# Performance work log

Hardware: AMD Instinct MI355X
Metric: run time of the kernel (lower is better)

Reference implementation:

```python
import jax, jax.numpy as jnp
import numpy as np

E = 8        # num_experts
D_IN = 512   # num_inputs
H = 256      # num_neurons_expert
T = 64       # num_neurons_tower
B = 16384    # batch


def setup_inputs() -> dict:
    key = jax.random.key(0)
    ks = jax.random.split(key, 7)
    s_in = 1.0 / np.sqrt(D_IN)
    s_h = 1.0 / np.sqrt(H)
    return {
        "xv": jax.random.normal(ks[0], (B, D_IN), dtype=jnp.float32),
        # expert weights stacked: torch Linear weight is (out,in) -> (E, H, D_IN)
        "We": jax.random.uniform(ks[1], (E, H, D_IN), jnp.float32, -s_in, s_in),
        "be": jax.random.uniform(ks[2], (E, H), jnp.float32, -s_in, s_in),
        "Wg": jax.random.uniform(ks[3], (E, D_IN), jnp.float32, -s_in, s_in),
        "bg": jax.random.uniform(ks[4], (E,), jnp.float32, -s_in, s_in),
        "Wt": jax.random.uniform(ks[5], (T, H), jnp.float32, -s_h, s_h),
        "bt": jax.random.uniform(ks[6], (T,), jnp.float32, -s_h, s_h),
    }


def reference(xv, We, be, Wg, bg, Wt, bt):
    # All experts as one batched GEMM: [B,D] x [E,H,D] -> [B,E,H]
    experts = jax.nn.relu(jnp.einsum("bd,ehd->beh", xv, We) + be[None, :, :])
    # Dropout is identity in eval mode.
    gate = jax.nn.softmax(xv @ Wg.T + bg, axis=1)            # [B,E]
    combined = jnp.einsum("beh,be->bh", experts, gate)        # [B,H]
    out = jax.nn.sigmoid(combined @ Wt.T + bt)                # [B,T]
    return out
```

## Files before the change

### kernel.cpp

```cpp
#include <hip/hip_runtime.h>
#include <hip/hip_bf16.h>
#include <stdint.h>

typedef unsigned short u16;
typedef __bf16 bf16x8 __attribute__((ext_vector_type(8)));
typedef float f32x4 __attribute__((ext_vector_type(4)));


__device__ __forceinline__ void glds16(const void* g, void* l) {
  __builtin_amdgcn_global_load_lds(
      (const __attribute__((address_space(1))) unsigned int*)g,
      (__attribute__((address_space(3))) unsigned int*)l, 16, 0, 0);
}

__device__ __forceinline__ u16 f2bf(float f) {
  unsigned int u = __builtin_bit_cast(unsigned int, f);
  u += 0x7fffu + ((u >> 16) & 1u);
  return (u16)(u >> 16);
}

__global__ __launch_bounds__(256) void prep_w(
    const float* __restrict__ We, const float* __restrict__ Wt,
    const float* __restrict__ Wg,
    u16* __restrict__ We_bf, u16* __restrict__ Wt_bf,
    u16* __restrict__ Wg_hi, u16* __restrict__ Wg_lo) {
  const int bx = blockIdx.x;
  if (bx < 520) {
    const float* src; u16* dst;
    if (bx < 512) { int base = bx * 2048 + threadIdx.x * 8; src = We + base; dst = We_bf + base; }
    else { int base = (bx - 512) * 2048 + threadIdx.x * 8; src = Wt + base; dst = Wt_bf + base; }
    float4 a = *(const float4*)src;
    float4 b = *(const float4*)(src + 4);
    uint4 o;
    o.x = (unsigned)f2bf(a.x) | ((unsigned)f2bf(a.y) << 16);
    o.y = (unsigned)f2bf(a.z) | ((unsigned)f2bf(a.w) << 16);
    o.z = (unsigned)f2bf(b.x) | ((unsigned)f2bf(b.y) << 16);
    o.w = (unsigned)f2bf(b.z) | ((unsigned)f2bf(b.w) << 16);
    *(uint4*)dst = o;
  } else {
    int base = (bx - 520) * 2048 + threadIdx.x * 8;
    float x[8];
    float4 a = *(const float4*)(Wg + base);
    float4 b = *(const float4*)(Wg + base + 4);
    x[0]=a.x; x[1]=a.y; x[2]=a.z; x[3]=a.w; x[4]=b.x; x[5]=b.y; x[6]=b.z; x[7]=b.w;
    u16 h[8], l[8];
#pragma unroll
    for (int j = 0; j < 8; j++) {
      h[j] = f2bf(x[j]);
      float hf = __builtin_bit_cast(float, ((unsigned)h[j]) << 16);
      l[j] = f2bf(x[j] - hf);
    }
    uint4 oh, ol;
    oh.x = (unsigned)h[0] | ((unsigned)h[1] << 16);
    oh.y = (unsigned)h[2] | ((unsigned)h[3] << 16);
    oh.z = (unsigned)h[4] | ((unsigned)h[5] << 16);
    oh.w = (unsigned)h[6] | ((unsigned)h[7] << 16);
    ol.x = (unsigned)l[0] | ((unsigned)l[1] << 16);
    ol.y = (unsigned)l[2] | ((unsigned)l[3] << 16);
    ol.z = (unsigned)l[4] | ((unsigned)l[5] << 16);
    ol.w = (unsigned)l[6] | ((unsigned)l[7] << 16);
    *(uint4*)(Wg_hi + base) = oh;
    *(uint4*)(Wg_lo + base) = ol;
  }
}

__device__ __forceinline__ void stage_chunk(const u16* __restrict__ We_bf,
                                            u16* ldsbuf, int t, int tid) {
  const int e_ = t >> 2, kc_ = t & 3;
  const u16* src = We_bf + (e_ << 17) + (kc_ << 7);
#pragma unroll
  for (int r = 0; r < 8; r++) {
    int gi = r * 512 + tid;
    int n = gi >> 4, s = gi & 15;
    int g = (s & 8) | ((s & 7) ^ (n & 7));
    glds16(src + (n << 9) + (g << 3), ldsbuf + (gi << 3));
  }
}

__global__ __launch_bounds__(512, 1) void moe_main(
    const float* __restrict__ xv, const u16* __restrict__ We_bf,
    const float* __restrict__ be, const float* __restrict__ bg,
    const u16* __restrict__ Wg_hi, const u16* __restrict__ Wg_lo,
    const u16* __restrict__ Wt_bf, const float* __restrict__ bt,
    float* __restrict__ out) {
  __shared__ u16 lds[65536];

  const int tid = threadIdx.x;
  const int lane = tid & 63;
  const int wid = tid >> 6;
  const int wm = wid >> 2;
  const int wn = wid & 3;
  const int l15 = lane & 15;
  const int l4 = lane >> 4;
  const int m0 = blockIdx.x << 6;

  stage_chunk(We_bf, lds, 0, tid);

  bf16x8 ah[2][16];
  f32x4 gacc[2] = {{0.f,0.f,0.f,0.f},{0.f,0.f,0.f,0.f}};
  const int esrc = l15 & 7;
#pragma unroll
  for (int mt = 0; mt < 2; mt++) {
#pragma unroll
    for (int ks = 0; ks < 16; ks++) {
      const float* ap = xv + ((m0 + wm * 32 + mt * 16 + l15) << 9) + ks * 32 + l4 * 8;
      float4 xa = *(const float4*)ap;
      float4 xb = *(const float4*)(ap + 4);
      float x[8];
      x[0]=xa.x; x[1]=xa.y; x[2]=xa.z; x[3]=xa.w; x[4]=xb.x; x[5]=xb.y; x[6]=xb.z; x[7]=xb.w;
      bf16x8 hv, lv;
#pragma unroll
      for (int j = 0; j < 8; j++) {
        u16 hb_ = f2bf(x[j]);
        float hf = __builtin_bit_cast(float, ((unsigned)hb_) << 16);
        hv[j] = __builtin_bit_cast(__bf16, hb_);
        lv[j] = __builtin_bit_cast(__bf16, f2bf(x[j] - hf));
      }
      ah[mt][ks] = hv;
      bf16x8 wh = *(const bf16x8*)(Wg_hi + (esrc << 9) + ks * 32 + l4 * 8);
      bf16x8 wl = *(const bf16x8*)(Wg_lo + (esrc << 9) + ks * 32 + l4 * 8);
      gacc[mt] = __builtin_amdgcn_mfma_f32_16x16x32_bf16(hv, wh, gacc[mt], 0, 0, 0);
      gacc[mt] = __builtin_amdgcn_mfma_f32_16x16x32_bf16(lv, wh, gacc[mt], 0, 0, 0);
      gacc[mt] = __builtin_amdgcn_mfma_f32_16x16x32_bf16(hv, wl, gacc[mt], 0, 0, 0);
    }
  }
  float gv[2][4];
  {
    float bgv = bg[esrc];
#pragma unroll
    for (int mt = 0; mt < 2; mt++)
#pragma unroll
      for (int i = 0; i < 4; i++) {
        float z = gacc[mt][i] + bgv;
        float mx = z;
        mx = fmaxf(mx, __shfl_xor(mx, 1));
        mx = fmaxf(mx, __shfl_xor(mx, 2));
        mx = fmaxf(mx, __shfl_xor(mx, 4));
        float p = __expf(z - mx);
        float s = p;
        s += __shfl_xor(s, 1);
        s += __shfl_xor(s, 2);
        s += __shfl_xor(s, 4);
        gv[mt][i] = p / s;
      }
  }

  f32x4 comb[2][4];
#pragma unroll
  for (int mt = 0; mt < 2; mt++)
#pragma unroll
    for (int nt = 0; nt < 4; nt++) comb[mt][nt] = {0.f, 0.f, 0.f, 0.f};

#pragma unroll 1
  for (int e = 0; e < 8; e++) {
    f32x4 acc[2][4];
#pragma unroll
    for (int mt = 0; mt < 2; mt++)
#pragma unroll
      for (int nt = 0; nt < 4; nt++) acc[mt][nt] = {0.f, 0.f, 0.f, 0.f};

#pragma unroll
    for (int kc = 0; kc < 4; kc++) {
      __syncthreads();
      int t = e * 4 + kc + 1;
      if (t < 32) stage_chunk(We_bf, &lds[(((kc & 1) ^ 1) << 15)], t, tid);
      const u16* ldsB = &lds[((kc & 1) << 15)];
#pragma unroll
      for (int ks = 0; ks < 4; ks++) {
        const int gg = ks * 4 + l4;
        bf16x8 bfr[4];
#pragma unroll
        for (int nt = 0; nt < 4; nt++) {
          int n = wn * 64 + nt * 16 + l15;
          int slot = (gg & 8) | ((gg & 7) ^ (n & 7));
          bfr[nt] = *(const bf16x8*)&ldsB[(n << 7) + (slot << 3)];
        }
#pragma unroll
        for (int mt = 0; mt < 2; mt++)
#pragma unroll
          for (int nt = 0; nt < 4; nt++)
            acc[mt][nt] = __builtin_amdgcn_mfma_f32_16x16x32_bf16(
                ah[mt][kc * 4 + ks], bfr[nt], acc[mt][nt], 0, 0, 0);
      }
    }
    float bev[4];
#pragma unroll
    for (int nt = 0; nt < 4; nt++)
      bev[nt] = be[(e << 8) + wn * 64 + nt * 16 + l15];
#pragma unroll
    for (int mt = 0; mt < 2; mt++)
#pragma unroll
      for (int i = 0; i < 4; i++) {
        float g = __shfl(gv[mt][i], (lane & 48) | e);
#pragma unroll
        for (int nt = 0; nt < 4; nt++)
          comb[mt][nt][i] += g * fmaxf(acc[mt][nt][i] + bev[nt], 0.f);
      }
  }

  __syncthreads();
#pragma unroll
  for (int mt = 0; mt < 2; mt++)
#pragma unroll
    for (int i = 0; i < 4; i++) {
      int row = wm * 32 + mt * 16 + l4 * 4 + i;
#pragma unroll
      for (int nt = 0; nt < 4; nt++) {
        int col = wn * 64 + nt * 16 + l15;
        __bf16 v = (__bf16)comb[mt][nt][i];
        lds[row * 264 + col] = __builtin_bit_cast(u16, v);
      }
    }
  __syncthreads();
  if (wid < 4) {
    f32x4 tacc[4];
#pragma unroll
    for (int nt = 0; nt < 4; nt++) tacc[nt] = {0.f, 0.f, 0.f, 0.f};
#pragma unroll
    for (int ks = 0; ks < 8; ks++) {
      bf16x8 aT = *(const bf16x8*)&lds[(wid * 16 + l15) * 264 + ks * 32 + l4 * 8];
#pragma unroll
      for (int nt = 0; nt < 4; nt++) {
        bf16x8 bT = *(const bf16x8*)&Wt_bf[(nt * 16 + l15) * 256 + ks * 32 + l4 * 8];
        tacc[nt] = __builtin_amdgcn_mfma_f32_16x16x32_bf16(aT, bT, tacc[nt], 0, 0, 0);
      }
    }
#pragma unroll
    for (int nt = 0; nt < 4; nt++) {
      float btv = bt[nt * 16 + l15];
#pragma unroll
      for (int i = 0; i < 4; i++) {
        int row = m0 + wid * 16 + l4 * 4 + i;
        float v = tacc[nt][i] + btv;
        out[row * 64 + nt * 16 + l15] = 1.f / (1.f + __expf(-v));
      }
    }
  }
}

extern "C" void kernel_launch(void* const* d_in, const int* in_sizes, int n_in,
                              void* d_out, int out_size, void* d_ws, size_t ws_size,
                              hipStream_t stream) {
  const float* xv = (const float*)d_in[0];
  const float* We = (const float*)d_in[1];
  const float* be = (const float*)d_in[2];
  const float* Wg = (const float*)d_in[3];
  const float* bg = (const float*)d_in[4];
  const float* Wt = (const float*)d_in[5];
  const float* bt = (const float*)d_in[6];

  char* ws = (char*)d_ws;
  u16* We_bf = (u16*)ws;
  u16* Wt_bf = (u16*)(ws + 2097152);
  u16* Wg_hi = (u16*)(ws + 2129920);
  u16* Wg_lo = (u16*)(ws + 2138112);

  prep_w<<<522, 256, 0, stream>>>(We, Wt, Wg, We_bf, Wt_bf, Wg_hi, Wg_lo);
  moe_main<<<256, 512, 0, stream>>>(xv, We_bf, be, bg, Wg_hi, Wg_lo, Wt_bf, bt,
                                    (float*)d_out);
}
```

Before: 157.6 us.

## Prefetch two weight chunks ahead with explicit waitcnt barriers, cache expert bias in LDS

Restructures the We chunk staging so each LDS buffer is refilled two chunks ahead, right after it is consumed. Explicit vmcnt waits and raw s_barriers replace the per-chunk __syncthreads, so global-to-LDS loads can overlap more MFMA work. The gate GEMM now uses three independent accumulators to break the MFMA dependency chain. The expert bias is also staged once into LDS instead of being read from global memory per expert. The hand-written waitcnt counts and the removal of the final sync carry a risk of race conditions if the counts are wrong.

```diff
diff --git a/kernel.cpp b/kernel.cpp
--- a/kernel.cpp
+++ b/kernel.cpp
@@ -6,6 +6,11 @@
 typedef __bf16 bf16x8 __attribute__((ext_vector_type(8)));
 typedef float f32x4 __attribute__((ext_vector_type(4)));
 
+
+#define SBAR __builtin_amdgcn_s_barrier()
+#define SCHEDB __builtin_amdgcn_sched_barrier(0)
+#define WAIT_V8 asm volatile("s_waitcnt vmcnt(8) lgkmcnt(0)" ::: "memory")
+#define WAIT_V0 asm volatile("s_waitcnt vmcnt(0) lgkmcnt(0)" ::: "memory")
 
 __device__ __forceinline__ void glds16(const void* g, void* l) {
   __builtin_amdgcn_global_load_lds(
@@ -83,7 +88,8 @@
     const u16* __restrict__ Wg_hi, const u16* __restrict__ Wg_lo,
     const u16* __restrict__ Wt_bf, const float* __restrict__ bt,
     float* __restrict__ out) {
-  __shared__ u16 lds[65536];
+  __shared__ u16 lds[69632];
+  float* beL = (float*)&lds[65536];
 
   const int tid = threadIdx.x;
   const int lane = tid & 63;
@@ -95,9 +101,13 @@
   const int m0 = blockIdx.x << 6;
 
   stage_chunk(We_bf, lds, 0, tid);
+  *(float4*)(beL + (tid << 2)) = *(const float4*)(be + (tid << 2));
+  stage_chunk(We_bf, &lds[32768], 1, tid);
 
   bf16x8 ah[2][16];
-  f32x4 gacc[2] = {{0.f,0.f,0.f,0.f},{0.f,0.f,0.f,0.f}};
+  f32x4 g0[2] = {{0.f,0.f,0.f,0.f},{0.f,0.f,0.f,0.f}};
+  f32x4 g1[2] = {{0.f,0.f,0.f,0.f},{0.f,0.f,0.f,0.f}};
+  f32x4 g2[2] = {{0.f,0.f,0.f,0.f},{0.f,0.f,0.f,0.f}};
   const int esrc = l15 & 7;
 #pragma unroll
   for (int mt = 0; mt < 2; mt++) {
@@ -119,9 +129,10 @@
       ah[mt][ks] = hv;
       bf16x8 wh = *(const bf16x8*)(Wg_hi + (esrc << 9) + ks * 32 + l4 * 8);
       bf16x8 wl = *(const bf16x8*)(Wg_lo + (esrc << 9) + ks * 32 + l4 * 8);
-      gacc[mt] = __builtin_amdgcn_mfma_f32_16x16x32_bf16(hv, wh, gacc[mt], 0, 0, 0);
-      gacc[mt] = __builtin_amdgcn_mfma_f32_16x16x32_bf16(lv, wh, gacc[mt], 0, 0, 0);
-      gacc[mt] = __builtin_amdgcn_mfma_f32_16x16x32_bf16(hv, wl, gacc[mt], 0, 0, 0);
+      g0[mt] = __builtin_amdgcn_mfma_f32_16x16x32_bf16(hv, wh, g0[mt], 0, 0, 0);
+      g1[mt] = __builtin_amdgcn_mfma_f32_16x16x32_bf16(lv, wh, g1[mt], 0, 0, 0);
+      g2[mt] = __builtin_amdgcn_mfma_f32_16x16x32_bf16(hv, wl, g2[mt], 0, 0, 0);
+      if ((ks & 3) == 3) SCHEDB;
     }
   }
   float gv[2][4];
@@ -131,7 +142,7 @@
     for (int mt = 0; mt < 2; mt++)
 #pragma unroll
       for (int i = 0; i < 4; i++) {
-        float z = gacc[mt][i] + bgv;
+        float z = g0[mt][i] + g1[mt][i] + g2[mt][i] + bgv;
         float mx = z;
         mx = fmaxf(mx, __shfl_xor(mx, 1));
         mx = fmaxf(mx, __shfl_xor(mx, 2));
@@ -144,6 +155,7 @@
         gv[mt][i] = p / s;
       }
   }
+  SCHEDB;
 
   f32x4 comb[2][4];
 #pragma unroll
@@ -161,10 +173,14 @@
 
 #pragma unroll
     for (int kc = 0; kc < 4; kc++) {
-      __syncthreads();
-      int t = e * 4 + kc + 1;
-      if (t < 32) stage_chunk(We_bf, &lds[(((kc & 1) ^ 1) << 15)], t, tid);
-      const u16* ldsB = &lds[((kc & 1) << 15)];
+      if (kc == 3) {
+        if (e == 7) { WAIT_V0; } else { WAIT_V8; }
+      } else {
+        WAIT_V8;
+      }
+      SBAR;
+      SCHEDB;
+      const u16* ldsB = &lds[(kc & 1) << 15];
 #pragma unroll
       for (int ks = 0; ks < 4; ks++) {
         const int gg = ks * 4 + l4;
@@ -182,11 +198,15 @@
             acc[mt][nt] = __builtin_amdgcn_mfma_f32_16x16x32_bf16(
                 ah[mt][kc * 4 + ks], bfr[nt], acc[mt][nt], 0, 0, 0);
       }
+      SBAR;
+      SCHEDB;
+      int t2 = e * 4 + kc + 2;
+      if (t2 < 32) stage_chunk(We_bf, &lds[(kc & 1) << 15], t2, tid);
     }
     float bev[4];
 #pragma unroll
     for (int nt = 0; nt < 4; nt++)
-      bev[nt] = be[(e << 8) + wn * 64 + nt * 16 + l15];
+      bev[nt] = beL[(e << 8) + wn * 64 + nt * 16 + l15];
 #pragma unroll
     for (int mt = 0; mt < 2; mt++)
 #pragma unroll
@@ -198,7 +218,6 @@
       }
   }
 
-  __syncthreads();
 #pragma unroll
   for (int mt = 0; mt < 2; mt++)
 #pragma unroll
```

Result: slower. 179.4 us (+13.9%).

## Halve row tile to 32 with 4 waves and 2 blocks per CU

Applied to the files above, without the earlier changes.

Each block now handles 32 rows with 256 threads instead of 64 rows with 512, and the launch doubles to 512 blocks, aiming for two co-resident blocks per CU. Expert weight chunks are staged in K=64 slices with a simpler swizzle, and the first two chunks are prefetched before the gating GEMM. Biases are cached in LDS, and the gating MFMA chain is split into three independent accumulators to shorten the dependency chain. The trade-off is that every row tile restreams the full expert weight set, so L2 read traffic for the weights doubles.

```diff
diff --git a/kernel.cpp b/kernel.cpp
--- a/kernel.cpp
+++ b/kernel.cpp
@@ -66,44 +66,49 @@
 
 __device__ __forceinline__ void stage_chunk(const u16* __restrict__ We_bf,
                                             u16* ldsbuf, int t, int tid) {
-  const int e_ = t >> 2, kc_ = t & 3;
-  const u16* src = We_bf + (e_ << 17) + (kc_ << 7);
+  const int e_ = t >> 3, kc_ = t & 7;
+  const u16* src = We_bf + (e_ << 17) + (kc_ << 6);
 #pragma unroll
   for (int r = 0; r < 8; r++) {
-    int gi = r * 512 + tid;
-    int n = gi >> 4, s = gi & 15;
-    int g = (s & 8) | ((s & 7) ^ (n & 7));
+    int gi = r * 256 + tid;
+    int n = gi >> 3, s = gi & 7;
+    int g = s ^ (n & 7);
     glds16(src + (n << 9) + (g << 3), ldsbuf + (gi << 3));
   }
 }
 
-__global__ __launch_bounds__(512, 1) void moe_main(
+__global__ __launch_bounds__(256, 2) void moe_main(
     const float* __restrict__ xv, const u16* __restrict__ We_bf,
     const float* __restrict__ be, const float* __restrict__ bg,
     const u16* __restrict__ Wg_hi, const u16* __restrict__ Wg_lo,
     const u16* __restrict__ Wt_bf, const float* __restrict__ bt,
     float* __restrict__ out) {
-  __shared__ u16 lds[65536];
+  __shared__ u16 lds[36864];
+  float* beL = (float*)&lds[32768];
 
   const int tid = threadIdx.x;
   const int lane = tid & 63;
   const int wid = tid >> 6;
-  const int wm = wid >> 2;
-  const int wn = wid & 3;
+  const int wn = wid;
   const int l15 = lane & 15;
   const int l4 = lane >> 4;
-  const int m0 = blockIdx.x << 6;
+  const int m0 = blockIdx.x << 5;
 
   stage_chunk(We_bf, lds, 0, tid);
+  *(float4*)(beL + (tid << 3)) = *(const float4*)(be + (tid << 3));
+  *(float4*)(beL + (tid << 3) + 4) = *(const float4*)(be + (tid << 3) + 4);
+  stage_chunk(We_bf, &lds[16384], 1, tid);
 
   bf16x8 ah[2][16];
-  f32x4 gacc[2] = {{0.f,0.f,0.f,0.f},{0.f,0.f,0.f,0.f}};
+  f32x4 g0[2] = {{0.f,0.f,0.f,0.f},{0.f,0.f,0.f,0.f}};
+  f32x4 g1[2] = {{0.f,0.f,0.f,0.f},{0.f,0.f,0.f,0.f}};
+  f32x4 g2[2] = {{0.f,0.f,0.f,0.f},{0.f,0.f,0.f,0.f}};
   const int esrc = l15 & 7;
 #pragma unroll
   for (int mt = 0; mt < 2; mt++) {
 #pragma unroll
     for (int ks = 0; ks < 16; ks++) {
-      const float* ap = xv + ((m0 + wm * 32 + mt * 16 + l15) << 9) + ks * 32 + l4 * 8;
+      const float* ap = xv + ((m0 + mt * 16 + l15) << 9) + ks * 32 + l4 * 8;
       float4 xa = *(const float4*)ap;
       float4 xb = *(const float4*)(ap + 4);
       float x[8];
@@ -119,9 +124,9 @@
       ah[mt][ks] = hv;
       bf16x8 wh = *(const bf16x8*)(Wg_hi + (esrc << 9) + ks * 32 + l4 * 8);
       bf16x8 wl = *(const bf16x8*)(Wg_lo + (esrc << 9) + ks * 32 + l4 * 8);
-      gacc[mt] = __builtin_amdgcn_mfma_f32_16x16x32_bf16(hv, wh, gacc[mt], 0, 0, 0);
-      gacc[mt] = __builtin_amdgcn_mfma_f32_16x16x32_bf16(lv, wh, gacc[mt], 0, 0, 0);
-      gacc[mt] = __builtin_amdgcn_mfma_f32_16x16x32_bf16(hv, wl, gacc[mt], 0, 0, 0);
+      g0[mt] = __builtin_amdgcn_mfma_f32_16x16x32_bf16(hv, wh, g0[mt], 0, 0, 0);
+      g1[mt] = __builtin_amdgcn_mfma_f32_16x16x32_bf16(lv, wh, g1[mt], 0, 0, 0);
+      g2[mt] = __builtin_amdgcn_mfma_f32_16x16x32_bf16(hv, wl, g2[mt], 0, 0, 0);
     }
   }
   float gv[2][4];
@@ -131,7 +136,7 @@
     for (int mt = 0; mt < 2; mt++)
 #pragma unroll
       for (int i = 0; i < 4; i++) {
-        float z = gacc[mt][i] + bgv;
+        float z = g0[mt][i] + g1[mt][i] + g2[mt][i] + bgv;
         float mx = z;
         mx = fmaxf(mx, __shfl_xor(mx, 1));
         mx = fmaxf(mx, __shfl_xor(mx, 2));
@@ -160,33 +165,34 @@
       for (int nt = 0; nt < 4; nt++) acc[mt][nt] = {0.f, 0.f, 0.f, 0.f};
 
 #pragma unroll
-    for (int kc = 0; kc < 4; kc++) {
+    for (int kc = 0; kc < 8; kc++) {
+      int t = e * 8 + kc;
       __syncthreads();
-      int t = e * 4 + kc + 1;
-      if (t < 32) stage_chunk(We_bf, &lds[(((kc & 1) ^ 1) << 15)], t, tid);
-      const u16* ldsB = &lds[((kc & 1) << 15)];
-#pragma unroll
-      for (int ks = 0; ks < 4; ks++) {
-        const int gg = ks * 4 + l4;
+      if (t + 1 >= 2 && t + 1 < 64)
+        stage_chunk(We_bf, &lds[((t & 1) ^ 1) << 14], t + 1, tid);
+      const u16* ldsB = &lds[(t & 1) << 14];
+#pragma unroll
+      for (int ks = 0; ks < 2; ks++) {
         bf16x8 bfr[4];
 #pragma unroll
         for (int nt = 0; nt < 4; nt++) {
           int n = wn * 64 + nt * 16 + l15;
-          int slot = (gg & 8) | ((gg & 7) ^ (n & 7));
-          bfr[nt] = *(const bf16x8*)&ldsB[(n << 7) + (slot << 3)];
+          int g = ks * 4 + l4;
+          int slot = g ^ (n & 7);
+          bfr[nt] = *(const bf16x8*)&ldsB[(n << 6) + (slot << 3)];
         }
 #pragma unroll
         for (int mt = 0; mt < 2; mt++)
 #pragma unroll
           for (int nt = 0; nt < 4; nt++)
             acc[mt][nt] = __builtin_amdgcn_mfma_f32_16x16x32_bf16(
-                ah[mt][kc * 4 + ks], bfr[nt], acc[mt][nt], 0, 0, 0);
+                ah[mt][kc * 2 + ks], bfr[nt], acc[mt][nt], 0, 0, 0);
       }
     }
     float bev[4];
 #pragma unroll
     for (int nt = 0; nt < 4; nt++)
-      bev[nt] = be[(e << 8) + wn * 64 + nt * 16 + l15];
+      bev[nt] = beL[(e << 8) + wn * 64 + nt * 16 + l15];
 #pragma unroll
     for (int mt = 0; mt < 2; mt++)
 #pragma unroll
@@ -198,12 +204,11 @@
       }
   }
 
-  __syncthreads();
 #pragma unroll
   for (int mt = 0; mt < 2; mt++)
 #pragma unroll
     for (int i = 0; i < 4; i++) {
-      int row = wm * 32 + mt * 16 + l4 * 4 + i;
+      int row = mt * 16 + l4 * 4 + i;
 #pragma unroll
       for (int nt = 0; nt < 4; nt++) {
         int col = wn * 64 + nt * 16 + l15;
@@ -212,7 +217,7 @@
       }
     }
   __syncthreads();
-  if (wid < 4) {
+  if (wid < 2) {
     f32x4 tacc[4];
 #pragma unroll
     for (int nt = 0; nt < 4; nt++) tacc[nt] = {0.f, 0.f, 0.f, 0.f};
@@ -256,6 +261,6 @@
   u16* Wg_lo = (u16*)(ws + 2138112);
 
   prep_w<<<522, 256, 0, stream>>>(We, Wt, Wg, We_bf, Wt_bf, Wg_hi, Wg_lo);
-  moe_main<<<256, 512, 0, stream>>>(xv, We_bf, be, bg, Wg_hi, Wg_lo, Wt_bf, bt,
+  moe_main<<<512, 256, 0, stream>>>(xv, We_bf, be, bg, Wg_hi, Wg_lo, Wt_bf, bt,
                                     (float*)d_out);
 }
```

Measured after the change: 177.9 us. 12.9% more time.
